# Kernel tuning notes

Measured on AMD Instinct MI355X. Metric: run time of the kernel, lower is better.

The kernel has to match this reference:

```python
import jax, jax.numpy as jnp
import numpy as np

N_NODES = 2048
N_GRAPHS = 64
N_EDGES = 16384
B = 65536
META = 64
TX = 8
NOISE = 128
IN_DIM = N_NODES + 1 + 32 + TX  # 2089


def setup_inputs() -> dict:
    key = jax.random.key(0)
    ks = jax.random.split(key, 11)
    return {
        "batched_graphs": jax.random.randint(ks[0], (B,), 0, N_GRAPHS),
        "batched_chain": jax.random.normal(ks[1], (B,), dtype=jnp.float32),
        "trigger_data": jax.random.normal(ks[2], (B, META), dtype=jnp.float32),
        "tx_start_time": jax.random.normal(ks[3], (B, TX), dtype=jnp.float32),
        "edges": jax.random.randint(ks[4], (N_GRAPHS, 2, N_EDGES), 0, N_NODES),
        "gcn_w": jax.random.normal(ks[5], (), dtype=jnp.float32),
        "gcn_b": jax.random.normal(ks[6], (), dtype=jnp.float32) * 0.01,
        "trig_W": jax.random.normal(ks[7], (META, 32), dtype=jnp.float32) / np.sqrt(META),
        "trig_b": jnp.zeros((32,), dtype=jnp.float32),
        "emb_W": jax.random.normal(ks[8], (IN_DIM, NOISE), dtype=jnp.float32) / np.sqrt(IN_DIM),
        "emb_b": jnp.zeros((NOISE,), dtype=jnp.float32),
    }


def _gcn_one_graph(edge_index, w, b):
    # GCNConv(1,1) on x = ones(n_nodes,1): add self loops, sym-normalize.
    self_idx = jnp.arange(N_NODES, dtype=edge_index.dtype)
    src = jnp.concatenate([edge_index[0], self_idx])
    dst = jnp.concatenate([edge_index[1], self_idx])
    deg = jax.ops.segment_sum(jnp.ones(src.shape[0], jnp.float32), dst,
                              num_segments=N_NODES)
    dinv = jnp.where(deg > 0, jax.lax.rsqrt(deg), 0.0)
    norm = dinv[src] * dinv[dst]
    agg = jax.ops.segment_sum(norm, dst, num_segments=N_NODES)  # [n_nodes]
    return agg * w + b  # x @ W with x==1 is just w per node, plus bias


def reference(batched_graphs, batched_chain, trigger_data, tx_start_time,
              edges, gcn_w, gcn_b, trig_W, trig_b, emb_W, emb_b):
    # Per-graph GCN embeddings for all topologies (covers all uniques). [G, n_nodes]
    graph_emb = jax.vmap(lambda e: _gcn_one_graph(e, gcn_w, gcn_b))(edges)
    ge = graph_emb[batched_graphs]                         # [B, n_nodes] gather
    trig = jax.nn.relu(trigger_data @ trig_W + trig_b)     # [B, 32]
    x = jnp.concatenate(
        [ge, batched_chain[:, None], trig, tx_start_time], axis=1)  # [B, IN_DIM]
    return x @ emb_W + emb_b                               # [B, NOISE]
```

## Files before the change

kernel.cpp:

```cpp
#include <hip/hip_runtime.h>

#define NN 2048
#define NG 64
#define NE 16384
#define BB 65536
#define META 64
#define TXD 8
#define NOISE 128


__global__ __launch_bounds__(256) void agg_kernel(
    const int* __restrict__ edges,
    const float* __restrict__ gcn_w,
    const float* __restrict__ gcn_b,
    float* __restrict__ emb,
    float* __restrict__ graph_out)
{
    __shared__ int   s_cnt[NN];
    __shared__ float s_dinv[NN];
    __shared__ float s_val[NN];
    const int g = blockIdx.x, tid = threadIdx.x;
    const int4* __restrict__ e4 = (const int4*)(edges + (size_t)g * 2 * NE);

    if (tid < NOISE) graph_out[g * NOISE + tid] = 0.0f;

    int4 ds[16];
    #pragma unroll
    for (int k = 0; k < 16; ++k) ds[k] = e4[4096 + k * 256 + tid];

    for (int n = tid; n < NN; n += 256) { s_cnt[n] = 1; s_val[n] = 0.0f; }
    __syncthreads();

    #pragma unroll
    for (int k = 0; k < 16; ++k) {
        atomicAdd(&s_cnt[ds[k].x], 1);
        atomicAdd(&s_cnt[ds[k].y], 1);
        atomicAdd(&s_cnt[ds[k].z], 1);
        atomicAdd(&s_cnt[ds[k].w], 1);
    }
    __syncthreads();
    for (int n = tid; n < NN; n += 256) s_dinv[n] = rsqrtf((float)s_cnt[n]);
    __syncthreads();

    #pragma unroll
    for (int k = 0; k < 16; ++k) {
        int4 sr = e4[k * 256 + tid];
        unsafeAtomicAdd(&s_val[ds[k].x], s_dinv[sr.x]);
        unsafeAtomicAdd(&s_val[ds[k].y], s_dinv[sr.y]);
        unsafeAtomicAdd(&s_val[ds[k].z], s_dinv[sr.z]);
        unsafeAtomicAdd(&s_val[ds[k].w], s_dinv[sr.w]);
    }
    __syncthreads();

    const float w = gcn_w[0], b = gcn_b[0];
    for (int n = tid; n < NN; n += 256) {
        float di = s_dinv[n];
        emb[(size_t)g * NN + n] = di * (s_val[n] + di) * w + b;
    }
}

__global__ __launch_bounds__(256) void fold_kernel(
    const float* __restrict__ emb,
    const float* __restrict__ emb_W,
    float* __restrict__ graph_out)
{
    __shared__ float s_e[128];
    __shared__ float s_red[128];
    const int tid = threadIdx.x;
    const int g = blockIdx.x >> 4, chunk = blockIdx.x & 15;
    const int n0 = chunk * 128;
    if (tid < 128) s_e[tid] = emb[(size_t)g * NN + n0 + tid];
    __syncthreads();
    const int c = tid & 127, h = tid >> 7;
    const float* __restrict__ Wp = emb_W + (size_t)(n0 + h * 64) * NOISE + c;
    const float* __restrict__ ep = s_e + h * 64;
    float a0 = 0.f, a1 = 0.f, a2 = 0.f, a3 = 0.f;
    #pragma unroll
    for (int i = 0; i < 64; i += 4) {
        a0 = fmaf(ep[i + 0], Wp[(i + 0) * NOISE], a0);
        a1 = fmaf(ep[i + 1], Wp[(i + 1) * NOISE], a1);
        a2 = fmaf(ep[i + 2], Wp[(i + 2) * NOISE], a2);
        a3 = fmaf(ep[i + 3], Wp[(i + 3) * NOISE], a3);
    }
    float acc = (a0 + a1) + (a2 + a3);
    if (h == 1) s_red[c] = acc;
    __syncthreads();
    if (h == 0) unsafeAtomicAdd(&graph_out[g * NOISE + c], acc + s_red[c]);
}

#define ROWS 32
__global__ __launch_bounds__(256, 3) void main_kernel(
    const int* __restrict__ bg,
    const float* __restrict__ chain,
    const float* __restrict__ trig_in,
    const float* __restrict__ txs,
    const float* __restrict__ trig_W,
    const float* __restrict__ trig_b,
    const float* __restrict__ emb_W,
    const float* __restrict__ emb_b,
    const float* __restrict__ graph_out,
    float* __restrict__ out)
{
    __shared__ float s_td[ROWS * 68];
    __shared__ float s_twT[32 * 68];
    __shared__ float s_trig[ROWS * 36];
    __shared__ float s_tx[ROWS * TXD];
    __shared__ float s_ch[ROWS];
    __shared__ int   s_gi[ROWS];

    const int tid = threadIdx.x;
    const int row0 = blockIdx.x * ROWS;

    {
        const float4* __restrict__ gsrc =
            (const float4*)(trig_in + (size_t)row0 * META);
        #pragma unroll
        for (int k = 0; k < 2; ++k) {
            int t = tid + k * 256;
            int r = t >> 4, i4 = t & 15;
            *(float4*)&s_td[r * 68 + i4 * 4] = gsrc[t];
        }
    }
    {
        const float4* __restrict__ gsrc = (const float4*)trig_W;
        #pragma unroll
        for (int k = 0; k < 2; ++k) {
            int t = tid + k * 256;
            int i = t >> 3, j4 = (t & 7) * 4;
            float4 v = gsrc[t];
            s_twT[(j4 + 0) * 68 + i] = v.x;
            s_twT[(j4 + 1) * 68 + i] = v.y;
            s_twT[(j4 + 2) * 68 + i] = v.z;
            s_twT[(j4 + 3) * 68 + i] = v.w;
        }
    }
    if (tid < 64) {
        int r = tid >> 1, k4 = (tid & 1) * 4;
        *(float4*)&s_tx[r * TXD + k4] =
            ((const float4*)(txs + (size_t)row0 * TXD))[tid];
    } else if (tid < 96) {
        int r = tid - 64;
        s_ch[r] = chain[row0 + r];
    } else if (tid < 128) {
        int r = tid - 96;
        s_gi[r] = bg[row0 + r];
    }

    const int n0 = (tid & 63) * 2;
    float2 w2[32], w3[TXD];
    #pragma unroll
    for (int j = 0; j < 32; ++j)
        w2[j] = *(const float2*)&emb_W[(size_t)(2049 + j) * NOISE + n0];
    #pragma unroll
    for (int k = 0; k < TXD; ++k)
        w3[k] = *(const float2*)&emb_W[(size_t)(2081 + k) * NOISE + n0];
    const float2 w1   = *(const float2*)&emb_W[(size_t)2048 * NOISE + n0];
    const float2 bias = *(const float2*)&emb_b[n0];

    __syncthreads();

    {
        const int j0 = tid & 15;
        const int r0 = (tid >> 4) * 2;
        const float* __restrict__ tw0 = s_twT + j0 * 68;
        const float* __restrict__ tw1 = s_twT + (j0 + 16) * 68;
        const float* __restrict__ td0 = s_td + r0 * 68;
        const float* __restrict__ td1 = s_td + (r0 + 1) * 68;
        float b0 = trig_b[j0], b1 = trig_b[j0 + 16];
        float a00 = b0, a01 = b1, a10 = b0, a11 = b1;
        #pragma unroll
        for (int i = 0; i < META; i += 4) {
            float4 u0 = *(const float4*)(tw0 + i);
            float4 u1 = *(const float4*)(tw1 + i);
            float4 t0 = *(const float4*)(td0 + i);
            float4 t1 = *(const float4*)(td1 + i);
            a00 = fmaf(t0.x, u0.x, a00); a00 = fmaf(t0.y, u0.y, a00);
            a00 = fmaf(t0.z, u0.z, a00); a00 = fmaf(t0.w, u0.w, a00);
            a01 = fmaf(t0.x, u1.x, a01); a01 = fmaf(t0.y, u1.y, a01);
            a01 = fmaf(t0.z, u1.z, a01); a01 = fmaf(t0.w, u1.w, a01);
            a10 = fmaf(t1.x, u0.x, a10); a10 = fmaf(t1.y, u0.y, a10);
            a10 = fmaf(t1.z, u0.z, a10); a10 = fmaf(t1.w, u0.w, a10);
            a11 = fmaf(t1.x, u1.x, a11); a11 = fmaf(t1.y, u1.y, a11);
            a11 = fmaf(t1.z, u1.z, a11); a11 = fmaf(t1.w, u1.w, a11);
        }
        s_trig[r0 * 36 + j0]            = fmaxf(a00, 0.f);
        s_trig[r0 * 36 + j0 + 16]       = fmaxf(a01, 0.f);
        s_trig[(r0 + 1) * 36 + j0]      = fmaxf(a10, 0.f);
        s_trig[(r0 + 1) * 36 + j0 + 16] = fmaxf(a11, 0.f);
    }
    __syncthreads();

    const int wv = tid >> 6;
    int   gs[8];
    float chs[8];
    #pragma unroll
    for (int p = 0; p < 8; ++p) {
        const int r = p * 4 + wv;
        gs[p]  = s_gi[r];
        chs[p] = s_ch[r];
    }
    float2 go[8];
    #pragma unroll
    for (int p = 0; p < 8; ++p)
        go[p] = *(const float2*)&graph_out[gs[p] * NOISE + n0];

    #pragma unroll
    for (int p = 0; p < 8; ++p) {
        const int r = p * 4 + wv;
        const int row = row0 + r;
        float ax = bias.x + go[p].x + chs[p] * w1.x;
        float ay = bias.y + go[p].y + chs[p] * w1.y;
        const float4* __restrict__ tx4 = (const float4*)(s_tx + r * TXD);
        float4 t0 = tx4[0], t1 = tx4[1];
        ax = fmaf(t0.x, w3[0].x, ax); ay = fmaf(t0.x, w3[0].y, ay);
        ax = fmaf(t0.y, w3[1].x, ax); ay = fmaf(t0.y, w3[1].y, ay);
        ax = fmaf(t0.z, w3[2].x, ax); ay = fmaf(t0.z, w3[2].y, ay);
        ax = fmaf(t0.w, w3[3].x, ax); ay = fmaf(t0.w, w3[3].y, ay);
        ax = fmaf(t1.x, w3[4].x, ax); ay = fmaf(t1.x, w3[4].y, ay);
        ax = fmaf(t1.y, w3[5].x, ax); ay = fmaf(t1.y, w3[5].y, ay);
        ax = fmaf(t1.z, w3[6].x, ax); ay = fmaf(t1.z, w3[6].y, ay);
        ax = fmaf(t1.w, w3[7].x, ax); ay = fmaf(t1.w, w3[7].y, ay);
        const float* __restrict__ tg = s_trig + r * 36;
        #pragma unroll
        for (int q = 0; q < 8; ++q) {
            float4 t4 = *(const float4*)(tg + q * 4);
            ax = fmaf(t4.x, w2[4 * q + 0].x, ax); ay = fmaf(t4.x, w2[4 * q + 0].y, ay);
            ax = fmaf(t4.y, w2[4 * q + 1].x, ax); ay = fmaf(t4.y, w2[4 * q + 1].y, ay);
            ax = fmaf(t4.z, w2[4 * q + 2].x, ax); ay = fmaf(t4.z, w2[4 * q + 2].y, ay);
            ax = fmaf(t4.w, w2[4 * q + 3].x, ax); ay = fmaf(t4.w, w2[4 * q + 3].y, ay);
        }
        *(float2*)&out[(size_t)row * NOISE + n0] = make_float2(ax, ay);
    }
}

extern "C" void kernel_launch(void* const* d_in, const int* in_sizes, int n_in,
                              void* d_out, int out_size, void* d_ws, size_t ws_size,
                              hipStream_t stream) {
    const int*   bg      = (const int*)d_in[0];
    const float* chain   = (const float*)d_in[1];
    const float* trig_in = (const float*)d_in[2];
    const float* txs     = (const float*)d_in[3];
    const int*   edges   = (const int*)d_in[4];
    const float* gcn_w   = (const float*)d_in[5];
    const float* gcn_b   = (const float*)d_in[6];
    const float* trig_W  = (const float*)d_in[7];
    const float* trig_b  = (const float*)d_in[8];
    const float* emb_W   = (const float*)d_in[9];
    const float* emb_b   = (const float*)d_in[10];
    float* out = (float*)d_out;

    float* graph_out = (float*)d_ws;
    float* emb       = (float*)d_ws + NG * NOISE;

    agg_kernel<<<NG, 256, 0, stream>>>(edges, gcn_w, gcn_b, emb, graph_out);
    fold_kernel<<<NG * 16, 256, 0, stream>>>(emb, emb_W, graph_out);
    main_kernel<<<BB / ROWS, 256, 0, stream>>>(bg, chain, trig_in, txs, trig_W,
                                               trig_b, emb_W, emb_b, graph_out, out);
}
```

Measured before the change: 145.4 us.

## Split per-graph GCN aggregation across four blocks per graph with partial buffers

The single-block-per-graph aggregation kernel is replaced by a degree kernel and an accumulation kernel. Each runs four blocks per graph, each block handling a quarter of the edges and writing partial degree or partial sum arrays to workspace. The fold kernel then combines the four partials and applies the GCN normalisation, weight and bias. The aim is to raise occupancy in the preprocessing phase, which previously ran only 64 blocks. The cost is an extra launch plus extra global traffic for the partial arrays.

```diff
diff --git a/kernel.cpp b/kernel.cpp
--- a/kernel.cpp
+++ b/kernel.cpp
@@ -9,58 +9,81 @@
 #define NOISE 128
 
 
-__global__ __launch_bounds__(256) void agg_kernel(
+__global__ __launch_bounds__(256) void deg_kernel(
     const int* __restrict__ edges,
-    const float* __restrict__ gcn_w,
-    const float* __restrict__ gcn_b,
-    float* __restrict__ emb,
+    int*   __restrict__ deg4,
     float* __restrict__ graph_out)
 {
-    __shared__ int   s_cnt[NN];
-    __shared__ float s_dinv[NN];
-    __shared__ float s_val[NN];
-    const int g = blockIdx.x, tid = threadIdx.x;
-    const int4* __restrict__ e4 = (const int4*)(edges + (size_t)g * 2 * NE);
-
-    if (tid < NOISE) graph_out[g * NOISE + tid] = 0.0f;
-
-    int4 ds[16];
-    #pragma unroll
-    for (int k = 0; k < 16; ++k) ds[k] = e4[4096 + k * 256 + tid];
-
-    for (int n = tid; n < NN; n += 256) { s_cnt[n] = 1; s_val[n] = 0.0f; }
-    __syncthreads();
-
-    #pragma unroll
-    for (int k = 0; k < 16; ++k) {
+    __shared__ int s_cnt[NN];
+    const int b = blockIdx.x, g = b >> 2, q = b & 3, tid = threadIdx.x;
+
+    if (q == 0 && tid < NOISE) graph_out[g * NOISE + tid] = 0.0f;
+
+    const int4* __restrict__ ed =
+        (const int4*)(edges + (size_t)g * 2 * NE + NE + q * 4096);
+    int4 ds[4];
+    #pragma unroll
+    for (int k = 0; k < 4; ++k) ds[k] = ed[k * 256 + tid];
+
+    for (int n = tid; n < NN; n += 256) s_cnt[n] = 0;
+    __syncthreads();
+    #pragma unroll
+    for (int k = 0; k < 4; ++k) {
         atomicAdd(&s_cnt[ds[k].x], 1);
         atomicAdd(&s_cnt[ds[k].y], 1);
         atomicAdd(&s_cnt[ds[k].z], 1);
         atomicAdd(&s_cnt[ds[k].w], 1);
     }
     __syncthreads();
-    for (int n = tid; n < NN; n += 256) s_dinv[n] = rsqrtf((float)s_cnt[n]);
-    __syncthreads();
-
-    #pragma unroll
-    for (int k = 0; k < 16; ++k) {
-        int4 sr = e4[k * 256 + tid];
-        unsafeAtomicAdd(&s_val[ds[k].x], s_dinv[sr.x]);
-        unsafeAtomicAdd(&s_val[ds[k].y], s_dinv[sr.y]);
-        unsafeAtomicAdd(&s_val[ds[k].z], s_dinv[sr.z]);
-        unsafeAtomicAdd(&s_val[ds[k].w], s_dinv[sr.w]);
-    }
-    __syncthreads();
-
-    const float w = gcn_w[0], b = gcn_b[0];
-    for (int n = tid; n < NN; n += 256) {
-        float di = s_dinv[n];
-        emb[(size_t)g * NN + n] = di * (s_val[n] + di) * w + b;
-    }
+    int* dp = deg4 + ((size_t)g * 4 + q) * NN;
+    for (int n = tid; n < NN; n += 256) dp[n] = s_cnt[n];
+}
+
+__global__ __launch_bounds__(256) void acc_kernel(
+    const int* __restrict__ edges,
+    const int* __restrict__ deg4,
+    float* __restrict__ acc4)
+{
+    __shared__ float s_dinv[NN];
+    __shared__ float s_val[NN];
+    const int b = blockIdx.x, g = b >> 2, q = b & 3, tid = threadIdx.x;
+
+    const int4* __restrict__ es =
+        (const int4*)(edges + (size_t)g * 2 * NE + q * 4096);
+    const int4* __restrict__ ed =
+        (const int4*)(edges + (size_t)g * 2 * NE + NE + q * 4096);
+    int4 ds[4], sr[4];
+    #pragma unroll
+    for (int k = 0; k < 4; ++k) ds[k] = ed[k * 256 + tid];
+    #pragma unroll
+    for (int k = 0; k < 4; ++k) sr[k] = es[k * 256 + tid];
+
+    {
+        const int* d0 = deg4 + (size_t)g * 4 * NN;
+        for (int n = tid; n < NN; n += 256) {
+            int d = d0[n] + d0[NN + n] + d0[2 * NN + n] + d0[3 * NN + n] + 1;
+            s_dinv[n] = rsqrtf((float)d);
+            s_val[n] = 0.0f;
+        }
+    }
+    __syncthreads();
+    #pragma unroll
+    for (int k = 0; k < 4; ++k) {
+        unsafeAtomicAdd(&s_val[ds[k].x], s_dinv[sr[k].x]);
+        unsafeAtomicAdd(&s_val[ds[k].y], s_dinv[sr[k].y]);
+        unsafeAtomicAdd(&s_val[ds[k].z], s_dinv[sr[k].z]);
+        unsafeAtomicAdd(&s_val[ds[k].w], s_dinv[sr[k].w]);
+    }
+    __syncthreads();
+    float* ap = acc4 + ((size_t)g * 4 + q) * NN;
+    for (int n = tid; n < NN; n += 256) ap[n] = s_val[n];
 }
 
 __global__ __launch_bounds__(256) void fold_kernel(
-    const float* __restrict__ emb,
+    const int* __restrict__ deg4,
+    const float* __restrict__ acc4,
+    const float* __restrict__ gcn_w,
+    const float* __restrict__ gcn_b,
     const float* __restrict__ emb_W,
     float* __restrict__ graph_out)
 {
@@ -69,7 +92,15 @@
     const int tid = threadIdx.x;
     const int g = blockIdx.x >> 4, chunk = blockIdx.x & 15;
     const int n0 = chunk * 128;
-    if (tid < 128) s_e[tid] = emb[(size_t)g * NN + n0 + tid];
+    if (tid < 128) {
+        const int n = n0 + tid;
+        const int* d0 = deg4 + (size_t)g * 4 * NN + n;
+        int d = d0[0] + d0[NN] + d0[2 * NN] + d0[3 * NN] + 1;
+        float di = rsqrtf((float)d);
+        const float* a0 = acc4 + (size_t)g * 4 * NN + n;
+        float sum = a0[0] + a0[NN] + a0[2 * NN] + a0[3 * NN];
+        s_e[tid] = di * (sum + di) * gcn_w[0] + gcn_b[0];
+    }
     __syncthreads();
     const int c = tid & 127, h = tid >> 7;
     const float* __restrict__ Wp = emb_W + (size_t)(n0 + h * 64) * NOISE + c;
@@ -249,11 +280,15 @@
     const float* emb_b   = (const float*)d_in[10];
     float* out = (float*)d_out;
 
-    float* graph_out = (float*)d_ws;
-    float* emb       = (float*)d_ws + NG * NOISE;
-
-    agg_kernel<<<NG, 256, 0, stream>>>(edges, gcn_w, gcn_b, emb, graph_out);
-    fold_kernel<<<NG * 16, 256, 0, stream>>>(emb, emb_W, graph_out);
+    float* wsf       = (float*)d_ws;
+    float* graph_out = wsf;
+    int*   deg4      = (int*)(wsf + 8192);
+    float* acc4      = wsf + 8192 + 524288;
+
+    deg_kernel<<<NG * 4, 256, 0, stream>>>(edges, deg4, graph_out);
+    acc_kernel<<<NG * 4, 256, 0, stream>>>(edges, deg4, acc4);
+    fold_kernel<<<NG * 16, 256, 0, stream>>>(deg4, acc4, gcn_w, gcn_b, emb_W,
+                                             graph_out);
     main_kernel<<<BB / ROWS, 256, 0, stream>>>(bg, chain, trig_in, txs, trig_W,
                                                trig_b, emb_W, emb_b, graph_out, out);
 }
```

After: 134.5 us. -7.5%, faster.
